# Performance work log

Hardware: AMD Instinct MI355X
Metric: run time of the kernel (lower is better)

## Reference

```python
import jax, jax.numpy as jnp
import numpy as np

# SuperposedExpert: K parallel TT-factorized FFN paths + holographic routing.
# d_model=1024 factorized as [32,32]; d_ff=4096 as [64,64]; tt_ranks=[1,16,1] (r0/r2 squeezed).
K, D_MODEL, D_FF, RANK = 4, 1024, 4096, 16
IN1, IN2 = 32, 32          # factorize_for_tt(d_model)
F1, F2 = 64, 64            # factorize_for_tt(d_ff)
TEMP = 1.0                 # routing_temperature


def setup_inputs() -> dict:
    key = jax.random.key(0)
    ks = jax.random.split(key, 8)
    s = 0.05
    tokens = jax.random.normal(ks[0], (2048, D_MODEL), dtype=jnp.float32)
    # TT cores for ffn1: d_model -> d_ff  (input_dims [32,32], output_dims [64,64])
    ffn1_core1 = jax.random.normal(ks[1], (K, IN1, F1, RANK), dtype=jnp.float32) * s
    ffn1_core2 = jax.random.normal(ks[2], (K, RANK, IN2, F2), dtype=jnp.float32) * s
    # TT cores for ffn2: d_ff -> d_model (input_dims [64,64], output_dims [32,32])
    ffn2_core1 = jax.random.normal(ks[3], (K, F1, IN1, RANK), dtype=jnp.float32) * s
    ffn2_core2 = jax.random.normal(ks[4], (K, RANK, F2, IN2), dtype=jnp.float32) * s
    # Holographic routing params (hd_dim == d_model -> identity HD projection)
    pb = jax.random.normal(ks[5], (K, D_MODEL), dtype=jnp.float32)
    path_bases = pb / jnp.linalg.norm(pb, axis=-1, keepdims=True)  # orthogonal-ish init
    path_weights = jax.random.normal(ks[6], (K, D_MODEL), dtype=jnp.float32) * s
    return {
        'tokens': tokens,
        'ffn1_core1': ffn1_core1, 'ffn1_core2': ffn1_core2,
        'ffn2_core1': ffn2_core1, 'ffn2_core2': ffn2_core2,
        'path_bases': path_bases, 'path_weights': path_weights,
    }


def reference(tokens, ffn1_core1, ffn1_core2, ffn2_core1, ffn2_core2,
              path_bases, path_weights):
    N = tokens.shape[0]
    # ---- K superposed TT-FFN paths ----
    x3 = tokens.reshape(N, IN1, IN2)  # [n, a, b]
    # TT matmul 1: y[x,y] = sum_{a,b,r} G1[a,x,r] G2[r,b,y] x[a,b]
    h = jnp.einsum('nab,kaxr,krby->knxy', x3, ffn1_core1, ffn1_core2)
    h = jax.nn.gelu(h.reshape(K, N, D_FF))  # quantum_activation stand-in
    h3 = h.reshape(K, N, F1, F2)
    y = jnp.einsum('knab,kaxr,krby->knxy', h3, ffn2_core1, ffn2_core2)
    y = y.reshape(K, N, D_MODEL)  # per-path outputs
    # ---- Holographic HD routing (hd_dim == d_model: identity projection) ----
    logits = jnp.einsum('nd,kd->nk', tokens, path_bases) / TEMP
    gates = jax.nn.softmax(logits, axis=-1)  # [n, k]
    # Collapse superposition: per-path elementwise HD modulation + gated sum
    out = jnp.einsum('knd,kd,nk->nd', y, 1.0 + path_weights, gates)
    return out
```

## Files before the change

### kernel.cpp

```cpp
#include <hip/hip_runtime.h>
#include <stdint.h>

#define GAS __attribute__((address_space(1)))
#define LAS __attribute__((address_space(3)))

typedef __attribute__((ext_vector_type(8))) short short8;
typedef __attribute__((ext_vector_type(16))) float f32x16;
typedef __attribute__((ext_vector_type(4))) float f32x4;

static constexpr int N_TOK = 2048;
static constexpr int DM    = 1024;
static constexpr int DF    = 4096;
static constexpr int KP    = 4;

__device__ inline unsigned short f2bf(float f) {
  union { float f; uint32_t u; } v; v.f = f;
  uint32_t u = v.u;
  u += 0x7FFFu + ((u >> 16) & 1u);
  return (unsigned short)(u >> 16);
}

__device__ inline uint32_t pk_bf(float lo, float hi) {
  union { float f; uint32_t u; } a, b; a.f = lo; b.f = hi;
  uint32_t ul = a.u + 0x7FFFu + ((a.u >> 16) & 1u);
  uint32_t uh = b.u + 0x7FFFu + ((b.u >> 16) & 1u);
  return (ul >> 16) | (uh & 0xFFFF0000u);
}

__device__ inline float gelu_gate(float v, float g) {
  float t0 = v * v;
  float u  = v * __builtin_fmaf(t0, -0.10294456f, -2.3022539f);
  float e  = __builtin_amdgcn_exp2f(u);
  float r  = __builtin_amdgcn_rcpf(1.0f + e);
  return v * g * r;
}

__device__ inline void gld16(const void* g, void* l) {
  __builtin_amdgcn_global_load_lds((const GAS void*)g, (LAS void*)l, 16, 0, 0);
}

__global__ __launch_bounds__(256) void setup_kernel(
    const float* __restrict__ tokens, const float* __restrict__ pb,
    const float* __restrict__ c11, const float* __restrict__ c12,
    const float* __restrict__ c21, const float* __restrict__ c22,
    float* __restrict__ gates, unsigned short* __restrict__ xb,
    unsigned short* __restrict__ w1t, unsigned short* __restrict__ w2t) {
  __shared__ __align__(16) float sh[17472];
  const int blk = blockIdx.x;
  const int t = threadIdx.x;
  if (blk < 1024) {
    const int k = blk >> 8, x = (blk >> 2) & 63, y0 = (blk & 3) * 16;
    float* s1  = sh;
    float* s2T = sh + 512;
    if (t < 128) {
      int a = t >> 2, rq = (t & 3) * 4;
      *(float4*)(s1 + a * 16 + rq) =
          *(const float4*)(c11 + (((size_t)(k * 32 + a)) * 64 + x) * 16 + rq);
    }
#pragma unroll
    for (int j = 0; j < 8; ++j) {
      int i = t + j * 256;
      int rb = i >> 2, yy0 = (i & 3) * 4;
      float4 v = *(const float4*)(c12 + (size_t)(k * 16) * 2048 + (size_t)rb * 64 + y0 + yy0);
      s2T[(yy0 + 0) * 524 + rb] = v.x;
      s2T[(yy0 + 1) * 524 + rb] = v.y;
      s2T[(yy0 + 2) * 524 + rb] = v.z;
      s2T[(yy0 + 3) * 524 + rb] = v.w;
    }
    __syncthreads();
    const int a = t >> 3, b0 = (t & 7) * 4;
    float4 s1q[4];
#pragma unroll
    for (int q = 0; q < 4; ++q) s1q[q] = *(const float4*)(s1 + a * 16 + q * 4);
    const float* a0s = (const float*)s1q;
    for (int y = 0; y < 16; ++y) {
      const float* s2y = s2T + y * 524;
      float4 acc = {0.f, 0.f, 0.f, 0.f};
#pragma unroll
      for (int r = 0; r < 16; ++r) {
        float cv = a0s[r];
        float4 bv = *(const float4*)(s2y + r * 32 + b0);
        acc.x = __builtin_fmaf(cv, bv.x, acc.x);
        acc.y = __builtin_fmaf(cv, bv.y, acc.y);
        acc.z = __builtin_fmaf(cv, bv.z, acc.z);
        acc.w = __builtin_fmaf(cv, bv.w, acc.w);
      }
      ushort4 o; o.x = f2bf(acc.x); o.y = f2bf(acc.y); o.z = f2bf(acc.z); o.w = f2bf(acc.w);
      *(ushort4*)(w1t + ((size_t)k * DF + x * 64 + y0 + y) * DM + t * 4) = o;
    }
  } else if (blk < 2048) {
    const int bb = blk - 1024;
    const int jj = bb & 3;
    const int rest = bb >> 2;
    const int k = rest >> 6, x = (rest >> 1) & 31, y0 = (rest & 1) * 16;
    float* s1  = sh;
    float* s2T = sh + 1024;
    {
      int a = t >> 2, rq = (t & 3) * 4;
      *(float4*)(s1 + a * 16 + rq) =
          *(const float4*)(c21 + (((size_t)(k * 64 + a)) * 32 + x) * 16 + rq);
    }
#pragma unroll
    for (int j = 0; j < 16; ++j) {
      int i = t + j * 256;
      int rb = i >> 2, yy0 = (i & 3) * 4;
      float4 v = *(const float4*)(c22 + (size_t)(k * 16) * 2048 + (size_t)rb * 32 + y0 + yy0);
      s2T[(yy0 + 0) * 1028 + rb] = v.x;
      s2T[(yy0 + 1) * 1028 + rb] = v.y;
      s2T[(yy0 + 2) * 1028 + rb] = v.z;
      s2T[(yy0 + 3) * 1028 + rb] = v.w;
    }
    __syncthreads();
    const int b0 = (t & 15) * 4;
    const int a = (t >> 4) + jj * 16;
    float4 s1q[4];
#pragma unroll
    for (int q = 0; q < 4; ++q) s1q[q] = *(const float4*)(s1 + a * 16 + q * 4);
    const float* a0s = (const float*)s1q;
    for (int y = 0; y < 16; ++y) {
      const float* s2y = s2T + y * 1028;
      float4 acc = {0.f, 0.f, 0.f, 0.f};
#pragma unroll
      for (int r = 0; r < 16; ++r) {
        float cv = a0s[r];
        float4 bv = *(const float4*)(s2y + r * 64 + b0);
        acc.x = __builtin_fmaf(cv, bv.x, acc.x);
        acc.y = __builtin_fmaf(cv, bv.y, acc.y);
        acc.z = __builtin_fmaf(cv, bv.z, acc.z);
        acc.w = __builtin_fmaf(cv, bv.w, acc.w);
      }
      ushort4 o; o.x = f2bf(acc.x); o.y = f2bf(acc.y); o.z = f2bf(acc.z); o.w = f2bf(acc.w);
      *(ushort4*)(w2t + ((size_t)k * DM + x * 32 + y0 + y) * DF + t * 4 + jj * 1024) = o;
    }
  } else {
    const int wave = t >> 6, lane = t & 63;
    const int n = (blk - 2048) * 4 + wave;
    float s0 = 0.f, s1v = 0.f, s2v = 0.f, s3v = 0.f;
    const float4* tr = (const float4*)(tokens + (size_t)n * DM);
#pragma unroll
    for (int j = 0; j < 4; ++j) {
      int idx = j * 64 + lane;
      float4 tv = tr[idx];
      ushort4 b;
      b.x = f2bf(tv.x); b.y = f2bf(tv.y); b.z = f2bf(tv.z); b.w = f2bf(tv.w);
      *(ushort4*)(xb + (size_t)n * DM + idx * 4) = b;
      float4 q;
      q = ((const float4*)(pb + 0 * DM))[idx]; s0  += tv.x*q.x + tv.y*q.y + tv.z*q.z + tv.w*q.w;
      q = ((const float4*)(pb + 1 * DM))[idx]; s1v += tv.x*q.x + tv.y*q.y + tv.z*q.z + tv.w*q.w;
      q = ((const float4*)(pb + 2 * DM))[idx]; s2v += tv.x*q.x + tv.y*q.y + tv.z*q.z + tv.w*q.w;
      q = ((const float4*)(pb + 3 * DM))[idx]; s3v += tv.x*q.x + tv.y*q.y + tv.z*q.z + tv.w*q.w;
    }
#pragma unroll
    for (int off = 32; off > 0; off >>= 1) {
      s0  += __shfl_xor(s0, off);
      s1v += __shfl_xor(s1v, off);
      s2v += __shfl_xor(s2v, off);
      s3v += __shfl_xor(s3v, off);
    }
    if (lane == 0) {
      float m = fmaxf(fmaxf(s0, s1v), fmaxf(s2v, s3v));
      float e0 = __expf(s0 - m), e1 = __expf(s1v - m), e2 = __expf(s2v - m), e3 = __expf(s3v - m);
      float inv = 1.0f / (e0 + e1 + e2 + e3);
      float4 g; g.x = e0 * inv; g.y = e1 * inv; g.z = e2 * inv; g.w = e3 * inv;
      *(float4*)(gates + n * 4) = g;
    }
  }
}

#define PH_SYNC(V) do { \
    asm volatile("s_waitcnt vmcnt(" #V ")" ::: "memory"); \
    __builtin_amdgcn_s_barrier(); \
    __builtin_amdgcn_sched_barrier(0); \
  } while (0)

#define G1_TILE(KT, BO, WO, V0, V1, V2) do { \
    const int kn_ = ((KT) + 1) * 64; \
    const bool st_ = (KT) < 15; \
     \
    PH_SYNC(V0); \
    if (st_) { const unsigned short* s_ = Wg + (size_t)srow * DM + kn_ + lch * 8; \
      gld16(s_, smem + (WO) + t * 16); gld16(s_ + 64 * DM, smem + (WO) + 8192 + t * 16); } \
    _Pragma("unroll") for (int fi = 0; fi < 4; ++fi) \
      _Pragma("unroll") for (int s = 0; s < 2; ++s) \
        af[fi][s] = *(const short8*)(smem + (BO) + aRowB + fi * 2048 + (cxor16 ^ (s * 64) ^ (fi * 32))); \
    _Pragma("unroll") for (int ti = 0; ti < 2; ++ti) \
      _Pragma("unroll") for (int s = 0; s < 2; ++s) \
        bf0[ti][s] = *(const short8*)(smem + (BO) + xRowB + ti * 2048 + (cxor16 ^ (s * 64) ^ wnx64 ^ (ti * 32))); \
    __builtin_amdgcn_s_setprio(1); \
    _Pragma("unroll") for (int fi = 0; fi < 4; ++fi) \
      _Pragma("unroll") for (int ti = 0; ti < 2; ++ti) { \
        acc[0][0][fi][ti] = __builtin_amdgcn_mfma_f32_16x16x32_bf16(af[fi][0], bf0[ti][0], acc[0][0][fi][ti], 0, 0, 0); \
        acc[0][0][fi][ti] = __builtin_amdgcn_mfma_f32_16x16x32_bf16(af[fi][1], bf0[ti][1], acc[0][0][fi][ti], 0, 0, 0); } \
    __builtin_amdgcn_s_setprio(0); \
     \
    PH_SYNC(V1); \
    if (st_) { const unsigned short* s_ = Xg + (size_t)srow * DM + kn_ + lch * 8; \
      gld16(s_, smem + (WO) + 32768 + t * 16); gld16(s_ + 64 * DM, smem + (WO) + 32768 + 8192 + t * 16); } \
    _Pragma("unroll") for (int ti = 0; ti < 2; ++ti) \
      _Pragma("unroll") for (int s = 0; s < 2; ++s) \
        bf1[ti][s] = *(const short8*)(smem + (BO) + xRowB + 16384 + ti * 2048 + (cxor16 ^ (s * 64) ^ wnx64 ^ (ti * 32))); \
    __builtin_amdgcn_s_setprio(1); \
    _Pragma("unroll") for (int fi = 0; fi < 4; ++fi) \
      _Pragma("unroll") for (int ti = 0; ti < 2; ++ti) { \
        acc[0][1][fi][ti] = __builtin_amdgcn_mfma_f32_16x16x32_bf16(af[fi][0], bf1[ti][0], acc[0][1][fi][ti], 0, 0, 0); \
        acc[0][1][fi][ti] = __builtin_amdgcn_mfma_f32_16x16x32_bf16(af[fi][1], bf1[ti][1], acc[0][1][fi][ti], 0, 0, 0); } \
    __builtin_amdgcn_s_setprio(0); \
     \
    PH_SYNC(V2); \
    if (st_) { const unsigned short* s_ = Xg + (size_t)(128 + srow) * DM + kn_ + lch * 8; \
      gld16(s_, smem + (WO) + 32768 + 16384 + t * 16); gld16(s_ + 64 * DM, smem + (WO) + 32768 + 16384 + 8192 + t * 16); } \
    _Pragma("unroll") for (int fi = 0; fi < 4; ++fi) \
      _Pragma("unroll") for (int s = 0; s < 2; ++s) \
        af[fi][s] = *(const short8*)(smem + (BO) + aRowB + 16384 + fi * 2048 + (cxor16 ^ (s * 64) ^ (fi * 32))); \
    __builtin_amdgcn_s_setprio(1); \
    _Pragma("unroll") for (int fi = 0; fi < 4; ++fi) \
      _Pragma("unroll") for (int ti = 0; ti < 2; ++ti) { \
        acc[1][1][fi][ti] = __builtin_amdgcn_mfma_f32_16x16x32_bf16(af[fi][0], bf1[ti][0], acc[1][1][fi][ti], 0, 0, 0); \
        acc[1][1][fi][ti] = __builtin_amdgcn_mfma_f32_16x16x32_bf16(af[fi][1], bf1[ti][1], acc[1][1][fi][ti], 0, 0, 0); } \
    __builtin_amdgcn_s_setprio(0); \
     \
    if (st_) { const unsigned short* s_ = Wg + (size_t)(128 + srow) * DM + kn_ + lch * 8; \
      gld16(s_, smem + (WO) + 16384 + t * 16); gld16(s_ + 64 * DM, smem + (WO) + 16384 + 8192 + t * 16); } \
    __builtin_amdgcn_s_setprio(1); \
    _Pragma("unroll") for (int fi = 0; fi < 4; ++fi) \
      _Pragma("unroll") for (int ti = 0; ti < 2; ++ti) { \
        acc[1][0][fi][ti] = __builtin_amdgcn_mfma_f32_16x16x32_bf16(af[fi][0], bf0[ti][0], acc[1][0][fi][ti], 0, 0, 0); \
        acc[1][0][fi][ti] = __builtin_amdgcn_mfma_f32_16x16x32_bf16(af[fi][1], bf0[ti][1], acc[1][0][fi][ti], 0, 0, 0); } \
    __builtin_amdgcn_s_setprio(0); \
  } while (0)

__global__ __launch_bounds__(512, 1) void gemm1(
    const unsigned short* __restrict__ xb, const unsigned short* __restrict__ w1t,
    const float* __restrict__ gates, unsigned short* __restrict__ hg) {
  __shared__ __align__(16) char smem[131072];
  const int t = threadIdx.x, lane = t & 63, wv = t >> 6;
  const int wm = wv >> 2, wn = wv & 3;
  const int hw = blockIdx.x + (blockIdx.y << 3) + (blockIdx.z << 7);
  const int lg = (hw & 7) * 64 + (hw >> 3);
  const int m0 = (lg & 7) * 256;
  const int f0 = ((lg >> 3) & 15) * 256;
  const int kp = lg >> 7;
  const unsigned short* __restrict__ Wg = w1t + (size_t)kp * DF * DM + (size_t)f0 * DM;
  const unsigned short* __restrict__ Xg = xb + (size_t)m0 * DM;

  const int srow = t >> 3;
  const int lch  = (t & 7) ^ (srow & 7) ^ (srow >> 3);
  const int l15 = lane & 15, kg = lane >> 4;
  const int cxor16 = (kg ^ (lane & 7) ^ (l15 >> 3)) * 16;
  const int wnx64  = (wn & 1) * 64;
  const int aRowB  = (wm * 64 + l15) * 128;
  const int xRowB  = 32768 + (wn * 32 + l15) * 128;

  f32x4 acc[2][2][4][2] = {};
  short8 af[4][2], bf0[2][2], bf1[2][2];

  {
    const unsigned short* sw = Wg + (size_t)srow * DM + lch * 8;
    const unsigned short* sx = Xg + (size_t)srow * DM + lch * 8;
    gld16(sw,            smem + t * 16);
    gld16(sw + 64 * DM,  smem + 8192 + t * 16);
    gld16(sx,            smem + 32768 + t * 16);
    gld16(sx + 64 * DM,  smem + 32768 + 8192 + t * 16);
    gld16(sx + 128 * DM, smem + 32768 + 16384 + t * 16);
    gld16(sx + 192 * DM, smem + 32768 + 16384 + 8192 + t * 16);
    gld16(sw + 128 * DM, smem + 16384 + t * 16);
    gld16(sw + 192 * DM, smem + 16384 + 8192 + t * 16);
  }

#pragma unroll 1
  for (int kt = 0; kt < 14; kt += 2) {
    G1_TILE(kt,     0,     65536, 4, 4, 4);
    G1_TILE(kt + 1, 65536, 0,     4, 4, 4);
  }
  G1_TILE(14, 0,     65536, 4, 4, 4);
  G1_TILE(15, 65536, 0,     4, 2, 0);

  unsigned short* __restrict__ H = hg + (size_t)kp * N_TOK * DF;
#pragma unroll
  for (int cB = 0; cB < 2; ++cB)
#pragma unroll
    for (int ti = 0; ti < 2; ++ti) {
      const int tok = m0 + cB * 128 + wn * 32 + ti * 16 + l15;
      const float g = gates[tok * 4 + kp];
      unsigned short* hrow = H + (size_t)tok * DF + f0 + wm * 64 + kg * 4;
#pragma unroll
      for (int rA = 0; rA < 2; ++rA)
#pragma unroll
        for (int fi = 0; fi < 4; ++fi) {
          f32x4 v = acc[rA][cB][fi][ti];
          float r0 = gelu_gate(v.x, g);
          float r1 = gelu_gate(v.y, g);
          float r2 = gelu_gate(v.z, g);
          float r3 = gelu_gate(v.w, g);
          uint2 p; p.x = pk_bf(r0, r1); p.y = pk_bf(r2, r3);
          *(uint2*)(hrow + rA * 128 + fi * 16) = p;
        }
    }
}

#define G2_TILE(KT, BO, WO, V0, V1, V2) do { \
    const int kn_ = ((KT) + 1) * 64; \
    const bool st_ = (KT) < 63; \
     \
    PH_SYNC(V0); \
    if (st_) gld16(Wg + (size_t)srow * DF + kn_ + lch * 8, smem + (WO) + t * 16); \
    _Pragma("unroll") for (int fi = 0; fi < 2; ++fi) \
      _Pragma("unroll") for (int s = 0; s < 2; ++s) \
        af[fi][s] = *(const short8*)(smem + (BO) + awRowB + fi * 2048 + (cxor16 ^ awx ^ (fi * 32) ^ (s * 64))); \
    _Pragma("unroll") for (int ti = 0; ti < 2; ++ti) \
      _Pragma("unroll") for (int s = 0; s < 2; ++s) \
        bf0[ti][s] = *(const short8*)(smem + (BO) + xRowB + ti * 2048 + (cxor16 ^ wnx64 ^ (ti * 32) ^ (s * 64))); \
    __builtin_amdgcn_s_setprio(1); \
    _Pragma("unroll") for (int fi = 0; fi < 2; ++fi) \
      _Pragma("unroll") for (int ti = 0; ti < 2; ++ti) { \
        acc[0][0][fi][ti] = __builtin_amdgcn_mfma_f32_16x16x32_bf16(af[fi][0], bf0[ti][0], acc[0][0][fi][ti], 0, 0, 0); \
        acc[0][0][fi][ti] = __builtin_amdgcn_mfma_f32_16x16x32_bf16(af[fi][1], bf0[ti][1], acc[0][0][fi][ti], 0, 0, 0); } \
    __builtin_amdgcn_s_setprio(0); \
     \
    PH_SYNC(V1); \
    if (st_) { const unsigned short* s_ = Xg + (size_t)srow * DF + kn_ + lch * 8; \
      gld16(s_, smem + (WO) + 16384 + t * 16); gld16(s_ + 64 * DF, smem + (WO) + 16384 + 8192 + t * 16); } \
    _Pragma("unroll") for (int ti = 0; ti < 2; ++ti) \
      _Pragma("unroll") for (int s = 0; s < 2; ++s) \
        bf1[ti][s] = *(const short8*)(smem + (BO) + xRowB + 16384 + ti * 2048 + (cxor16 ^ wnx64 ^ (ti * 32) ^ (s * 64))); \
    __builtin_amdgcn_s_setprio(1); \
    _Pragma("unroll") for (int fi = 0; fi < 2; ++fi) \
      _Pragma("unroll") for (int ti = 0; ti < 2; ++ti) { \
        acc[0][1][fi][ti] = __builtin_amdgcn_mfma_f32_16x16x32_bf16(af[fi][0], bf1[ti][0], acc[0][1][fi][ti], 0, 0, 0); \
        acc[0][1][fi][ti] = __builtin_amdgcn_mfma_f32_16x16x32_bf16(af[fi][1], bf1[ti][1], acc[0][1][fi][ti], 0, 0, 0); } \
    __builtin_amdgcn_s_setprio(0); \
     \
    PH_SYNC(V2); \
    if (st_) { const unsigned short* s_ = Xg + (size_t)(128 + srow) * DF + kn_ + lch * 8; \
      gld16(s_, smem + (WO) + 32768 + t * 16); gld16(s_ + 64 * DF, smem + (WO) + 32768 + 8192 + t * 16); } \
    _Pragma("unroll") for (int fi = 0; fi < 2; ++fi) \
      _Pragma("unroll") for (int s = 0; s < 2; ++s) \
        af[fi][s] = *(const short8*)(smem + (BO) + awRowB + 8192 + fi * 2048 + (cxor16 ^ awx ^ (fi * 32) ^ (s * 64))); \
    __builtin_amdgcn_s_setprio(1); \
    _Pragma("unroll") for (int fi = 0; fi < 2; ++fi) \
      _Pragma("unroll") for (int ti = 0; ti < 2; ++ti) { \
        acc[1][1][fi][ti] = __builtin_amdgcn_mfma_f32_16x16x32_bf16(af[fi][0], bf1[ti][0], acc[1][1][fi][ti], 0, 0, 0); \
        acc[1][1][fi][ti] = __builtin_amdgcn_mfma_f32_16x16x32_bf16(af[fi][1], bf1[ti][1], acc[1][1][fi][ti], 0, 0, 0); } \
    __builtin_amdgcn_s_setprio(0); \
     \
    if (st_) gld16(Wg + (size_t)(64 + srow) * DF + kn_ + lch * 8, smem + (WO) + 8192 + t * 16); \
    __builtin_amdgcn_s_setprio(1); \
    _Pragma("unroll") for (int fi = 0; fi < 2; ++fi) \
      _Pragma("unroll") for (int ti = 0; ti < 2; ++ti) { \
        acc[1][0][fi][ti] = __builtin_amdgcn_mfma_f32_16x16x32_bf16(af[fi][0], bf0[ti][0], acc[1][0][fi][ti], 0, 0, 0); \
        acc[1][0][fi][ti] = __builtin_amdgcn_mfma_f32_16x16x32_bf16(af[fi][1], bf0[ti][1], acc[1][0][fi][ti], 0, 0, 0); } \
    __builtin_amdgcn_s_setprio(0); \
  } while (0)

__global__ __launch_bounds__(512, 1) void gemm2(
    const unsigned short* __restrict__ hg, const unsigned short* __restrict__ w2t,
    const float* __restrict__ pw, float* __restrict__ part) {
  __shared__ __align__(16) char smem[98304];
  const int t = threadIdx.x, lane = t & 63, wv = t >> 6;
  const int wm = wv >> 2, wn = wv & 3;
  const int hw = blockIdx.x + (blockIdx.y << 3) + (blockIdx.z << 6);
  const int lg = (hw & 7) * 32 + (hw >> 3);
  const int m0 = (lg & 7) * 256;
  const int n0 = ((lg >> 3) & 7) * 128;
  const int kp = lg >> 6;
  const unsigned short* __restrict__ Wg = w2t + (size_t)kp * DM * DF + (size_t)n0 * DF;
  const unsigned short* __restrict__ Xg = hg + (size_t)kp * N_TOK * DF + (size_t)m0 * DF;

  const int srow = t >> 3;
  const int lch  = (t & 7) ^ (srow & 7) ^ (srow >> 3);
  const int l15 = lane & 15, kg = lane >> 4;
  const int cxor16 = (kg ^ (lane & 7) ^ (l15 >> 3)) * 16;
  const int wnx64  = (wn & 1) * 64;
  const int awx    = wm * 64;
  const int awRowB = (wm * 32 + l15) * 128;
  const int xRowB  = 16384 + (wn * 32 + l15) * 128;

  f32x4 acc[2][2][2][2] = {};
  short8 af[2][2], bf0[2][2], bf1[2][2];

  {
    const unsigned short* sw = Wg + (size_t)srow * DF + lch * 8;
    const unsigned short* sx = Xg + (size_t)srow * DF + lch * 8;
    gld16(sw,            smem + t * 16);
    gld16(sx,            smem + 16384 + t * 16);
    gld16(sx + 64 * DF,  smem + 16384 + 8192 + t * 16);
    gld16(sx + 128 * DF, smem + 32768 + t * 16);
    gld16(sx + 192 * DF, smem + 32768 + 8192 + t * 16);
    gld16(sw + 64 * DF,  smem + 8192 + t * 16);
  }

#pragma unroll 1
  for (int kt = 0; kt < 62; kt += 2) {
    G2_TILE(kt,     0,     49152, 3, 2, 3);
    G2_TILE(kt + 1, 49152, 0,     3, 2, 3);
  }
  G2_TILE(62, 0,     49152, 3, 2, 3);
  G2_TILE(63, 49152, 0,     3, 1, 0);

  float* __restrict__ P = part + (size_t)kp * N_TOK * DM;
  float4 pwv[2][2];
#pragma unroll
  for (int rA = 0; rA < 2; ++rA)
#pragma unroll
    for (int fi = 0; fi < 2; ++fi) {
      float4 w = *(const float4*)(pw + kp * DM + n0 + rA * 64 + wm * 32 + fi * 16 + kg * 4);
      pwv[rA][fi].x = 1.0f + w.x; pwv[rA][fi].y = 1.0f + w.y;
      pwv[rA][fi].z = 1.0f + w.z; pwv[rA][fi].w = 1.0f + w.w;
    }
#pragma unroll
  for (int cB = 0; cB < 2; ++cB)
#pragma unroll
    for (int ti = 0; ti < 2; ++ti) {
      const int tok = m0 + cB * 128 + wn * 32 + ti * 16 + l15;
      float* prow = P + (size_t)tok * DM + n0 + wm * 32 + kg * 4;
#pragma unroll
      for (int rA = 0; rA < 2; ++rA)
#pragma unroll
        for (int fi = 0; fi < 2; ++fi) {
          f32x4 v = acc[rA][cB][fi][ti];
          float4 o;
          o.x = pwv[rA][fi].x * v.x;
          o.y = pwv[rA][fi].y * v.y;
          o.z = pwv[rA][fi].z * v.z;
          o.w = pwv[rA][fi].w * v.w;
          *(float4*)(prow + rA * 64 + fi * 16) = o;
        }
    }
}

__global__ __launch_bounds__(256) void reduce_k(
    const float* __restrict__ part, float* __restrict__ out) {
  const size_t i = ((size_t)blockIdx.x * 256 + threadIdx.x) * 4;
  const size_t S = (size_t)N_TOK * DM;
  float4 a = *(const float4*)(part + i);
  float4 b = *(const float4*)(part + S + i);
  float4 c = *(const float4*)(part + 2 * S + i);
  float4 d = *(const float4*)(part + 3 * S + i);
  float4 r;
  r.x = a.x + b.x + c.x + d.x;
  r.y = a.y + b.y + c.y + d.y;
  r.z = a.z + b.z + c.z + d.z;
  r.w = a.w + b.w + c.w + d.w;
  *(float4*)(out + i) = r;
}

extern "C" void kernel_launch(void* const* d_in, const int* in_sizes, int n_in,
                              void* d_out, int out_size, void* d_ws, size_t ws_size,
                              hipStream_t stream) {
  const float* tokens = (const float*)d_in[0];
  const float* f1c1   = (const float*)d_in[1];
  const float* f1c2   = (const float*)d_in[2];
  const float* f2c1   = (const float*)d_in[3];
  const float* f2c2   = (const float*)d_in[4];
  const float* pb     = (const float*)d_in[5];
  const float* pw     = (const float*)d_in[6];
  float* out = (float*)d_out;

  char* ws = (char*)d_ws;
  unsigned short* xb  = (unsigned short*)(ws);
  unsigned short* w1t = (unsigned short*)(ws + (4ull  << 20));
  float*          part = (float*)(ws + (4ull << 20));
  unsigned short* w2t = (unsigned short*)(ws + (36ull << 20));
  unsigned short* hg  = (unsigned short*)(ws + (68ull << 20));
  float*          gates = (float*)(ws + (132ull << 20));

  hipLaunchKernelGGL(setup_kernel, dim3(2560), dim3(256), 0, stream,
                     tokens, pb, f1c1, f1c2, f2c1, f2c2, gates, xb, w1t, w2t);
  hipLaunchKernelGGL(gemm1, dim3(8, 16, KP), dim3(512), 0, stream, xb, w1t, gates, hg);
  hipLaunchKernelGGL(gemm2, dim3(8, 8, KP), dim3(512), 0, stream, hg, w2t, pw, part);
  hipLaunchKernelGGL(reduce_k, dim3(2048), dim3(256), 0, stream, part, out);
}
```

Before: 244.9 us.

## Switch both GEMMs from 16x16x32 to 32x32x16 bf16 MFMA tiles

```diff
diff --git a/kernel.cpp b/kernel.cpp
--- a/kernel.cpp
+++ b/kernel.cpp
@@ -180,52 +180,46 @@
     PH_SYNC(V0); \
     if (st_) { const unsigned short* s_ = Wg + (size_t)srow * DM + kn_ + lch * 8; \
       gld16(s_, smem + (WO) + t * 16); gld16(s_ + 64 * DM, smem + (WO) + 8192 + t * 16); } \
-    _Pragma("unroll") for (int fi = 0; fi < 4; ++fi) \
-      _Pragma("unroll") for (int s = 0; s < 2; ++s) \
-        af[fi][s] = *(const short8*)(smem + (BO) + aRowB + fi * 2048 + (cxor16 ^ (s * 64) ^ (fi * 32))); \
-    _Pragma("unroll") for (int ti = 0; ti < 2; ++ti) \
-      _Pragma("unroll") for (int s = 0; s < 2; ++s) \
-        bf0[ti][s] = *(const short8*)(smem + (BO) + xRowB + ti * 2048 + (cxor16 ^ (s * 64) ^ wnx64 ^ (ti * 32))); \
-    __builtin_amdgcn_s_setprio(1); \
-    _Pragma("unroll") for (int fi = 0; fi < 4; ++fi) \
-      _Pragma("unroll") for (int ti = 0; ti < 2; ++ti) { \
-        acc[0][0][fi][ti] = __builtin_amdgcn_mfma_f32_16x16x32_bf16(af[fi][0], bf0[ti][0], acc[0][0][fi][ti], 0, 0, 0); \
-        acc[0][0][fi][ti] = __builtin_amdgcn_mfma_f32_16x16x32_bf16(af[fi][1], bf0[ti][1], acc[0][0][fi][ti], 0, 0, 0); } \
+    _Pragma("unroll") for (int mi = 0; mi < 2; ++mi) \
+      _Pragma("unroll") for (int ks = 0; ks < 4; ++ks) \
+        af[mi][ks] = *(const short8*)(smem + (BO) + aRowB + mi * 4096 + (((ks * 2) ^ cxA ^ (mi * 4)) & 7) * 16); \
+    _Pragma("unroll") for (int ks = 0; ks < 4; ++ks) \
+        bf0[ks] = *(const short8*)(smem + (BO) + xRowB + (((ks * 2) ^ cxB) & 7) * 16); \
+    __builtin_amdgcn_s_setprio(1); \
+    _Pragma("unroll") for (int mi = 0; mi < 2; ++mi) \
+      _Pragma("unroll") for (int ks = 0; ks < 4; ++ks) \
+        acc[0][0][mi] = __builtin_amdgcn_mfma_f32_32x32x16_bf16(af[mi][ks], bf0[ks], acc[0][0][mi], 0, 0, 0); \
     __builtin_amdgcn_s_setprio(0); \
      \
     PH_SYNC(V1); \
     if (st_) { const unsigned short* s_ = Xg + (size_t)srow * DM + kn_ + lch * 8; \
       gld16(s_, smem + (WO) + 32768 + t * 16); gld16(s_ + 64 * DM, smem + (WO) + 32768 + 8192 + t * 16); } \
-    _Pragma("unroll") for (int ti = 0; ti < 2; ++ti) \
-      _Pragma("unroll") for (int s = 0; s < 2; ++s) \
-        bf1[ti][s] = *(const short8*)(smem + (BO) + xRowB + 16384 + ti * 2048 + (cxor16 ^ (s * 64) ^ wnx64 ^ (ti * 32))); \
-    __builtin_amdgcn_s_setprio(1); \
-    _Pragma("unroll") for (int fi = 0; fi < 4; ++fi) \
-      _Pragma("unroll") for (int ti = 0; ti < 2; ++ti) { \
-        acc[0][1][fi][ti] = __builtin_amdgcn_mfma_f32_16x16x32_bf16(af[fi][0], bf1[ti][0], acc[0][1][fi][ti], 0, 0, 0); \
-        acc[0][1][fi][ti] = __builtin_amdgcn_mfma_f32_16x16x32_bf16(af[fi][1], bf1[ti][1], acc[0][1][fi][ti], 0, 0, 0); } \
+    _Pragma("unroll") for (int ks = 0; ks < 4; ++ks) \
+        bf1[ks] = *(const short8*)(smem + (BO) + xRowB + 16384 + (((ks * 2) ^ cxB) & 7) * 16); \
+    __builtin_amdgcn_s_setprio(1); \
+    _Pragma("unroll") for (int mi = 0; mi < 2; ++mi) \
+      _Pragma("unroll") for (int ks = 0; ks < 4; ++ks) \
+        acc[0][1][mi] = __builtin_amdgcn_mfma_f32_32x32x16_bf16(af[mi][ks], bf1[ks], acc[0][1][mi], 0, 0, 0); \
     __builtin_amdgcn_s_setprio(0); \
      \
     PH_SYNC(V2); \
     if (st_) { const unsigned short* s_ = Xg + (size_t)(128 + srow) * DM + kn_ + lch * 8; \
       gld16(s_, smem + (WO) + 32768 + 16384 + t * 16); gld16(s_ + 64 * DM, smem + (WO) + 32768 + 16384 + 8192 + t * 16); } \
-    _Pragma("unroll") for (int fi = 0; fi < 4; ++fi) \
-      _Pragma("unroll") for (int s = 0; s < 2; ++s) \
-        af[fi][s] = *(const short8*)(smem + (BO) + aRowB + 16384 + fi * 2048 + (cxor16 ^ (s * 64) ^ (fi * 32))); \
-    __builtin_amdgcn_s_setprio(1); \
-    _Pragma("unroll") for (int fi = 0; fi < 4; ++fi) \
-      _Pragma("unroll") for (int ti = 0; ti < 2; ++ti) { \
-        acc[1][1][fi][ti] = __builtin_amdgcn_mfma_f32_16x16x32_bf16(af[fi][0], bf1[ti][0], acc[1][1][fi][ti], 0, 0, 0); \
-        acc[1][1][fi][ti] = __builtin_amdgcn_mfma_f32_16x16x32_bf16(af[fi][1], bf1[ti][1], acc[1][1][fi][ti], 0, 0, 0); } \
+    _Pragma("unroll") for (int mi = 0; mi < 2; ++mi) \
+      _Pragma("unroll") for (int ks = 0; ks < 4; ++ks) \
+        af[mi][ks] = *(const short8*)(smem + (BO) + aRowB + 16384 + mi * 4096 + (((ks * 2) ^ cxA ^ (mi * 4)) & 7) * 16); \
+    __builtin_amdgcn_s_setprio(1); \
+    _Pragma("unroll") for (int mi = 0; mi < 2; ++mi) \
+      _Pragma("unroll") for (int ks = 0; ks < 4; ++ks) \
+        acc[1][1][mi] = __builtin_amdgcn_mfma_f32_32x32x16_bf16(af[mi][ks], bf1[ks], acc[1][1][mi], 0, 0, 0); \
     __builtin_amdgcn_s_setprio(0); \
      \
     if (st_) { const unsigned short* s_ = Wg + (size_t)(128 + srow) * DM + kn_ + lch * 8; \
       gld16(s_, smem + (WO) + 16384 + t * 16); gld16(s_ + 64 * DM, smem + (WO) + 16384 + 8192 + t * 16); } \
     __builtin_amdgcn_s_setprio(1); \
-    _Pragma("unroll") for (int fi = 0; fi < 4; ++fi) \
-      _Pragma("unroll") for (int ti = 0; ti < 2; ++ti) { \
-        acc[1][0][fi][ti] = __builtin_amdgcn_mfma_f32_16x16x32_bf16(af[fi][0], bf0[ti][0], acc[1][0][fi][ti], 0, 0, 0); \
-        acc[1][0][fi][ti] = __builtin_amdgcn_mfma_f32_16x16x32_bf16(af[fi][1], bf0[ti][1], acc[1][0][fi][ti], 0, 0, 0); } \
+    _Pragma("unroll") for (int mi = 0; mi < 2; ++mi) \
+      _Pragma("unroll") for (int ks = 0; ks < 4; ++ks) \
+        acc[1][0][mi] = __builtin_amdgcn_mfma_f32_32x32x16_bf16(af[mi][ks], bf0[ks], acc[1][0][mi], 0, 0, 0); \
     __builtin_amdgcn_s_setprio(0); \
   } while (0)
 
@@ -245,14 +239,15 @@
 
   const int srow = t >> 3;
   const int lch  = (t & 7) ^ (srow & 7) ^ (srow >> 3);
-  const int l15 = lane & 15, kg = lane >> 4;
-  const int cxor16 = (kg ^ (lane & 7) ^ (l15 >> 3)) * 16;
-  const int wnx64  = (wn & 1) * 64;
-  const int aRowB  = (wm * 64 + l15) * 128;
-  const int xRowB  = 32768 + (wn * 32 + l15) * 128;
-
-  f32x4 acc[2][2][4][2] = {};
-  short8 af[4][2], bf0[2][2], bf1[2][2];
+  const int l31 = lane & 31, khalf = lane >> 5;
+  const int rsw = (l31 & 7) ^ (l31 >> 3);
+  const int cxA = khalf ^ rsw;
+  const int cxB = khalf ^ rsw ^ ((wn & 1) * 4);
+  const int aRowB = (wm * 64 + l31) * 128;
+  const int xRowB = 32768 + (wn * 32 + l31) * 128;
+
+  f32x16 acc[2][2][2] = {};
+  short8 af[2][4], bf0[4], bf1[4];
 
   {
     const unsigned short* sw = Wg + (size_t)srow * DM + lch * 8;
@@ -277,25 +272,26 @@
 
   unsigned short* __restrict__ H = hg + (size_t)kp * N_TOK * DF;
 #pragma unroll
-  for (int cB = 0; cB < 2; ++cB)
-#pragma unroll
-    for (int ti = 0; ti < 2; ++ti) {
-      const int tok = m0 + cB * 128 + wn * 32 + ti * 16 + l15;
-      const float g = gates[tok * 4 + kp];
-      unsigned short* hrow = H + (size_t)tok * DF + f0 + wm * 64 + kg * 4;
-#pragma unroll
-      for (int rA = 0; rA < 2; ++rA)
-#pragma unroll
-        for (int fi = 0; fi < 4; ++fi) {
-          f32x4 v = acc[rA][cB][fi][ti];
-          float r0 = gelu_gate(v.x, g);
-          float r1 = gelu_gate(v.y, g);
-          float r2 = gelu_gate(v.z, g);
-          float r3 = gelu_gate(v.w, g);
+  for (int cB = 0; cB < 2; ++cB) {
+    const int tok = m0 + cB * 128 + wn * 32 + l31;
+    const float g = gates[tok * 4 + kp];
+    unsigned short* hrow = H + (size_t)tok * DF + f0 + wm * 64 + khalf * 4;
+#pragma unroll
+    for (int rA = 0; rA < 2; ++rA)
+#pragma unroll
+      for (int mi = 0; mi < 2; ++mi) {
+        f32x16 v = acc[rA][cB][mi];
+#pragma unroll
+        for (int gq = 0; gq < 4; ++gq) {
+          float r0 = gelu_gate(v[gq * 4 + 0], g);
+          float r1 = gelu_gate(v[gq * 4 + 1], g);
+          float r2 = gelu_gate(v[gq * 4 + 2], g);
+          float r3 = gelu_gate(v[gq * 4 + 3], g);
           uint2 p; p.x = pk_bf(r0, r1); p.y = pk_bf(r2, r3);
-          *(uint2*)(hrow + rA * 128 + fi * 16) = p;
+          *(uint2*)(hrow + rA * 128 + mi * 32 + gq * 8) = p;
         }
-    }
+      }
+  }
 }
 
 #define G2_TILE(KT, BO, WO, V0, V1, V2) do { \
@@ -304,51 +300,39 @@
      \
     PH_SYNC(V0); \
     if (st_) gld16(Wg + (size_t)srow * DF + kn_ + lch * 8, smem + (WO) + t * 16); \
-    _Pragma("unroll") for (int fi = 0; fi < 2; ++fi) \
-      _Pragma("unroll") for (int s = 0; s < 2; ++s) \
-        af[fi][s] = *(const short8*)(smem + (BO) + awRowB + fi * 2048 + (cxor16 ^ awx ^ (fi * 32) ^ (s * 64))); \
-    _Pragma("unroll") for (int ti = 0; ti < 2; ++ti) \
-      _Pragma("unroll") for (int s = 0; s < 2; ++s) \
-        bf0[ti][s] = *(const short8*)(smem + (BO) + xRowB + ti * 2048 + (cxor16 ^ wnx64 ^ (ti * 32) ^ (s * 64))); \
-    __builtin_amdgcn_s_setprio(1); \
-    _Pragma("unroll") for (int fi = 0; fi < 2; ++fi) \
-      _Pragma("unroll") for (int ti = 0; ti < 2; ++ti) { \
-        acc[0][0][fi][ti] = __builtin_amdgcn_mfma_f32_16x16x32_bf16(af[fi][0], bf0[ti][0], acc[0][0][fi][ti], 0, 0, 0); \
-        acc[0][0][fi][ti] = __builtin_amdgcn_mfma_f32_16x16x32_bf16(af[fi][1], bf0[ti][1], acc[0][0][fi][ti], 0, 0, 0); } \
+    _Pragma("unroll") for (int ks = 0; ks < 4; ++ks) \
+        af[ks] = *(const short8*)(smem + (BO) + awRowB + (((ks * 2) ^ cxA) & 7) * 16); \
+    _Pragma("unroll") for (int ks = 0; ks < 4; ++ks) \
+        bf0[ks] = *(const short8*)(smem + (BO) + xRowB + (((ks * 2) ^ cxB) & 7) * 16); \
+    __builtin_amdgcn_s_setprio(1); \
+    _Pragma("unroll") for (int ks = 0; ks < 4; ++ks) \
+        acc[0][0] = __builtin_amdgcn_mfma_f32_32x32x16_bf16(af[ks], bf0[ks], acc[0][0], 0, 0, 0); \
     __builtin_amdgcn_s_setprio(0); \
      \
     PH_SYNC(V1); \
     if (st_) { const unsigned short* s_ = Xg + (size_t)srow * DF + kn_ + lch * 8; \
       gld16(s_, smem + (WO) + 16384 + t * 16); gld16(s_ + 64 * DF, smem + (WO) + 16384 + 8192 + t * 16); } \
-    _Pragma("unroll") for (int ti = 0; ti < 2; ++ti) \
-      _Pragma("unroll") for (int s = 0; s < 2; ++s) \
-        bf1[ti][s] = *(const short8*)(smem + (BO) + xRowB + 16384 + ti * 2048 + (cxor16 ^ wnx64 ^ (ti * 32) ^ (s * 64))); \
-    __builtin_amdgcn_s_setprio(1); \
-    _Pragma("unroll") for (int fi = 0; fi < 2; ++fi) \
-      _Pragma("unroll") for (int ti = 0; ti < 2; ++ti) { \
-        acc[0][1][fi][ti] = __builtin_amdgcn_mfma_f32_16x16x32_bf16(af[fi][0], bf1[ti][0], acc[0][1][fi][ti], 0, 0, 0); \
-        acc[0][1][fi][ti] = __builtin_amdgcn_mfma_f32_16x16x32_bf16(af[fi][1], bf1[ti][1], acc[0][1][fi][ti], 0, 0, 0); } \
+    _Pragma("unroll") for (int ks = 0; ks < 4; ++ks) \
+        bf1[ks] = *(const short8*)(smem + (BO) + xRowB + 16384 + (((ks * 2) ^ cxB) & 7) * 16); \
+    __builtin_amdgcn_s_setprio(1); \
+    _Pragma("unroll") for (int ks = 0; ks < 4; ++ks) \
+        acc[0][1] = __builtin_amdgcn_mfma_f32_32x32x16_bf16(af[ks], bf1[ks], acc[0][1], 0, 0, 0); \
     __builtin_amdgcn_s_setprio(0); \
      \
     PH_SYNC(V2); \
     if (st_) { const unsigned short* s_ = Xg + (size_t)(128 + srow) * DF + kn_ + lch * 8; \
       gld16(s_, smem + (WO) + 32768 + t * 16); gld16(s_ + 64 * DF, smem + (WO) + 32768 + 8192 + t * 16); } \
-    _Pragma("unroll") for (int fi = 0; fi < 2; ++fi) \
-      _Pragma("unroll") for (int s = 0; s < 2; ++s) \
-        af[fi][s] = *(const short8*)(smem + (BO) + awRowB + 8192 + fi * 2048 + (cxor16 ^ awx ^ (fi * 32) ^ (s * 64))); \
-    __builtin_amdgcn_s_setprio(1); \
-    _Pragma("unroll") for (int fi = 0; fi < 2; ++fi) \
-      _Pragma("unroll") for (int ti = 0; ti < 2; ++ti) { \
-        acc[1][1][fi][ti] = __builtin_amdgcn_mfma_f32_16x16x32_bf16(af[fi][0], bf1[ti][0], acc[1][1][fi][ti], 0, 0, 0); \
-        acc[1][1][fi][ti] = __builtin_amdgcn_mfma_f32_16x16x32_bf16(af[fi][1], bf1[ti][1], acc[1][1][fi][ti], 0, 0, 0); } \
+    _Pragma("unroll") for (int ks = 0; ks < 4; ++ks) \
+        af[ks] = *(const short8*)(smem + (BO) + awRowB + 8192 + (((ks * 2) ^ cxA) & 7) * 16); \
+    __builtin_amdgcn_s_setprio(1); \
+    _Pragma("unroll") for (int ks = 0; ks < 4; ++ks) \
+        acc[1][1] = __builtin_amdgcn_mfma_f32_32x32x16_bf16(af[ks], bf1[ks], acc[1][1], 0, 0, 0); \
     __builtin_amdgcn_s_setprio(0); \
      \
     if (st_) gld16(Wg + (size_t)(64 + srow) * DF + kn_ + lch * 8, smem + (WO) + 8192 + t * 16); \
     __builtin_amdgcn_s_setprio(1); \
-    _Pragma("unroll") for (int fi = 0; fi < 2; ++fi) \
-      _Pragma("unroll") for (int ti = 0; ti < 2; ++ti) { \
-        acc[1][0][fi][ti] = __builtin_amdgcn_mfma_f32_16x16x32_bf16(af[fi][0], bf0[ti][0], acc[1][0][fi][ti], 0, 0, 0); \
-        acc[1][0][fi][ti] = __builtin_amdgcn_mfma_f32_16x16x32_bf16(af[fi][1], bf0[ti][1], acc[1][0][fi][ti], 0, 0, 0); } \
+    _Pragma("unroll") for (int ks = 0; ks < 4; ++ks) \
+        acc[1][0] = __builtin_amdgcn_mfma_f32_32x32x16_bf16(af[ks], bf0[ks], acc[1][0], 0, 0, 0); \
     __builtin_amdgcn_s_setprio(0); \
   } while (0)
 
@@ -368,15 +352,15 @@
 
   const int srow = t >> 3;
   const int lch  = (t & 7) ^ (srow & 7) ^ (srow >> 3);
-  const int l15 = lane & 15, kg = lane >> 4;
-  const int cxor16 = (kg ^ (lane & 7) ^ (l15 >> 3)) * 16;
-  const int wnx64  = (wn & 1) * 64;
-  const int awx    = wm * 64;
-  const int awRowB = (wm * 32 + l15) * 128;
-  const int xRowB  = 16384 + (wn * 32 + l15) * 128;
-
-  f32x4 acc[2][2][2][2] = {};
-  short8 af[2][2], bf0[2][2], bf1[2][2];
+  const int l31 = lane & 31, khalf = lane >> 5;
+  const int rsw = (l31 & 7) ^ (l31 >> 3);
+  const int cxA = khalf ^ rsw ^ (wm * 4);
+  const int cxB = khalf ^ rsw ^ ((wn & 1) * 4);
+  const int awRowB = (wm * 32 + l31) * 128;
+  const int xRowB  = 16384 + (wn * 32 + l31) * 128;
+
+  f32x16 acc[2][2] = {};
+  short8 af[4], bf0[4], bf1[4];
 
   {
     const unsigned short* sw = Wg + (size_t)srow * DF + lch * 8;
@@ -398,34 +382,33 @@
   G2_TILE(63, 49152, 0,     3, 1, 0);
 
   float* __restrict__ P = part + (size_t)kp * N_TOK * DM;
-  float4 pwv[2][2];
+  float4 pwv[2][4];
 #pragma unroll
   for (int rA = 0; rA < 2; ++rA)
 #pragma unroll
-    for (int fi = 0; fi < 2; ++fi) {
-      float4 w = *(const float4*)(pw + kp * DM + n0 + rA * 64 + wm * 32 + fi * 16 + kg * 4);
-      pwv[rA][fi].x = 1.0f + w.x; pwv[rA][fi].y = 1.0f + w.y;
-      pwv[rA][fi].z = 1.0f + w.z; pwv[rA][fi].w = 1.0f + w.w;
-    }
-#pragma unroll
-  for (int cB = 0; cB < 2; ++cB)
-#pragma unroll
-    for (int ti = 0; ti < 2; ++ti) {
-      const int tok = m0 + cB * 128 + wn * 32 + ti * 16 + l15;
-      float* prow = P + (size_t)tok * DM + n0 + wm * 32 + kg * 4;
-#pragma unroll
-      for (int rA = 0; rA < 2; ++rA)
-#pragma unroll
-        for (int fi = 0; fi < 2; ++fi) {
-          f32x4 v = acc[rA][cB][fi][ti];
-          float4 o;
-          o.x = pwv[rA][fi].x * v.x;
-          o.y = pwv[rA][fi].y * v.y;
-          o.z = pwv[rA][fi].z * v.z;
-          o.w = pwv[rA][fi].w * v.w;
-          *(float4*)(prow + rA * 64 + fi * 16) = o;
-        }
-    }
+    for (int gq = 0; gq < 4; ++gq) {
+      float4 w = *(const float4*)(pw + kp * DM + n0 + rA * 64 + wm * 32 + khalf * 4 + gq * 8);
+      pwv[rA][gq].x = 1.0f + w.x; pwv[rA][gq].y = 1.0f + w.y;
+      pwv[rA][gq].z = 1.0f + w.z; pwv[rA][gq].w = 1.0f + w.w;
+    }
+#pragma unroll
+  for (int cB = 0; cB < 2; ++cB) {
+    const int tok = m0 + cB * 128 + wn * 32 + l31;
+    float* prow = P + (size_t)tok * DM + n0 + wm * 32 + khalf * 4;
+#pragma unroll
+    for (int rA = 0; rA < 2; ++rA) {
+      f32x16 v = acc[rA][cB];
+#pragma unroll
+      for (int gq = 0; gq < 4; ++gq) {
+        float4 o;
+        o.x = pwv[rA][gq].x * v[gq * 4 + 0];
+        o.y = pwv[rA][gq].y * v[gq * 4 + 1];
+        o.z = pwv[rA][gq].z * v[gq * 4 + 2];
+        o.w = pwv[rA][gq].w * v[gq * 4 + 3];
+        *(float4*)(prow + rA * 64 + gq * 8) = o;
+      }
+    }
+  }
 }
 
 __global__ __launch_bounds__(256) void reduce_k(
```

Result: slower. 259.6 us (+6.0%).
